# Kernel optimization log

Hardware: AMD Instinct MI355X
Metric: run time of the kernel (lower is better)

## Reference

```python
import jax, jax.numpy as jnp
import numpy as np

EPS_LN = 1e-5


def fwht(x):
    """Fast Walsh-Hadamard transform over the last axis (power-of-two length).
    Vectorized butterfly: log2(n) stages, each a reshape + add/sub."""
    orig_shape = x.shape
    n = orig_shape[-1]
    y = x.reshape(-1, n)
    h = 1
    while h < n:
        y = y.reshape(-1, n // (2 * h), 2, h)
        a = y[:, :, 0, :]
        b = y[:, :, 1, :]
        y = jnp.stack([a + b, a - b], axis=2).reshape(-1, n)
        h <<= 1
    return y.reshape(orig_shape)


def setup_inputs() -> dict:
    key = jax.random.key(0)
    kx, kw, kg = jax.random.split(key, 3)
    B, S, D_IN, D_OUT = 4, 4096, 2048, 2048
    x = jax.random.normal(kx, (B, S, D_IN), dtype=jnp.float32)
    # kaiming_uniform_(a=sqrt(5)) -> bound = 1/sqrt(in_features)
    bound = 1.0 / np.sqrt(D_IN)
    W = jax.random.uniform(kw, (D_OUT, D_IN), dtype=jnp.float32,
                           minval=-bound, maxval=bound)
    gamma = jnp.ones((D_IN,), dtype=jnp.float32)
    beta = jnp.zeros((D_IN,), dtype=jnp.float32)
    return {"x": x, "W": W, "gamma": gamma, "beta": beta}


def reference(x, W, gamma, beta):
    bits = 4
    max_val = (1 << (bits - 1)) - 1  # 7
    # LayerNorm over last dim
    mu = jnp.mean(x, axis=-1, keepdims=True)
    var = jnp.mean(jnp.square(x - mu), axis=-1, keepdims=True)
    x_ln = (x - mu) * jax.lax.rsqrt(var + EPS_LN) * gamma + beta
    # Activation fake-quant to `bits` bits (per-row absmax scale)
    x_scale = jnp.clip(jnp.max(jnp.abs(x_ln), axis=-1, keepdims=True), 1e-6, None)
    x_int = jnp.clip(jnp.round(x_ln * max_val / x_scale), -max_val, max_val)
    x_q = x_int * x_scale / max_val
    # Hadamard transform of quantized activations
    x_h = fwht(x_q)
    # Ternary weight quantization with global mean-abs scale
    w_scale = jnp.clip(jnp.mean(jnp.abs(W)), 1e-6, None)
    w_q = (jnp.where(W > 0.5 * w_scale, 1.0, 0.0)
           + jnp.where(W < -0.5 * w_scale, -1.0, 0.0)) * w_scale
    # Linear (no bias), then second Hadamard transform
    out = jnp.einsum('bsd,od->bso', x_h, w_q)
    return fwht(out)
```

## Files before the change

### kernel.cpp

```cpp
#include <hip/hip_runtime.h>

typedef unsigned short u16;
typedef __attribute__((ext_vector_type(8))) __bf16 bf16x8;
typedef __attribute__((ext_vector_type(4))) float floatx4;

#define DDIM 2048
#define MROWS 16384
#define BK 64

__device__ __forceinline__ u16 f2bf(float f) {
    unsigned int u = __builtin_bit_cast(unsigned int, f);
    u = (u + 0x7fffu + ((u >> 16) & 1u)) >> 16;
    return (u16)u;
}

__device__ __forceinline__ float wave_sum(float v) {
#pragma unroll
    for (int o = 32; o > 0; o >>= 1) v += __shfl_down(v, o, 64);
    return v;
}
__device__ __forceinline__ float wave_max(float v) {
#pragma unroll
    for (int o = 32; o > 0; o >>= 1) v = fmaxf(v, __shfl_down(v, o, 64));
    return v;
}

__global__ __launch_bounds__(256) void absmean_part(const float4* __restrict__ W4,
                                                    float* __restrict__ partial) {
    float s = 0.f;
    for (int i = blockIdx.x * 256 + threadIdx.x; i < (DDIM * DDIM / 4); i += 256 * 256) {
        float4 v = W4[i];
        s += fabsf(v.x) + fabsf(v.y) + fabsf(v.z) + fabsf(v.w);
    }
    s = wave_sum(s);
    __shared__ float red[4];
    if ((threadIdx.x & 63) == 0) red[threadIdx.x >> 6] = s;
    __syncthreads();
    if (threadIdx.x == 0) partial[blockIdx.x] = red[0] + red[1] + red[2] + red[3];
}

__global__ __launch_bounds__(256) void absmean_final(const float* __restrict__ partial,
                                                     float* __restrict__ scal) {
    float s = partial[threadIdx.x];
    s = wave_sum(s);
    __shared__ float red[4];
    if ((threadIdx.x & 63) == 0) red[threadIdx.x >> 6] = s;
    __syncthreads();
    if (threadIdx.x == 0) {
        float m = (red[0] + red[1] + red[2] + red[3]) * (1.0f / (float)(DDIM * DDIM));
        m = fmaxf(m, 1e-6f);
        scal[0] = m;
        scal[1] = 0.5f * m;
    }
}

template <bool QUANT>
__global__ __launch_bounds__(256) void transpose_k(const float* __restrict__ in,
                                                   float* __restrict__ out,
                                                   const float* __restrict__ scal) {
    __shared__ float tile[64][65];
    float wsc = 0.f, half_t = 0.f;
    if (QUANT) { wsc = scal[0]; half_t = scal[1]; }
    const int tx = threadIdx.x & 63;
    const int ty = threadIdx.x >> 6;
    const int r0 = blockIdx.y * 64;
    const int c0 = blockIdx.x * 64;
#pragma unroll
    for (int i = 0; i < 16; ++i) {
        int r = ty + i * 4;
        float w = in[(size_t)(r0 + r) * DDIM + c0 + tx];
        if (QUANT) w = (w > half_t ? wsc : 0.f) + (w < -half_t ? -wsc : 0.f);
        tile[r][tx] = w;
    }
    __syncthreads();
#pragma unroll
    for (int i = 0; i < 16; ++i) {
        int r = ty + i * 4;
        out[(size_t)(c0 + r) * DDIM + r0 + tx] = tile[tx][r];
    }
}

template <bool BF16OUT>
__global__ __launch_bounds__(256) void fwht_rows(const float* __restrict__ in,
                                                 void* __restrict__ out) {
    __shared__ float s0[DDIM];
    __shared__ float s1[DDIM];
    const int row = blockIdx.x;
    const int t = threadIdx.x;
    const int lane = t & 63;
    const float4* rp = (const float4*)(in + (size_t)row * DDIM);
    float4 a = rp[2 * t], b = rp[2 * t + 1];
    float v[8] = {a.x, a.y, a.z, a.w, b.x, b.y, b.z, b.w};

#pragma unroll
    for (int h = 1; h <= 4; h <<= 1)
#pragma unroll
        for (int j = 0; j < 8; ++j)
            if (!(j & h)) { float x = v[j], y = v[j | h]; v[j] = x + y; v[j | h] = x - y; }

#pragma unroll
    for (int m = 1; m <= 32; m <<= 1)
#pragma unroll
        for (int j = 0; j < 8; ++j) {
            float p = __shfl_xor(v[j], m, 64);
            v[j] = (lane & m) ? (p - v[j]) : (p + v[j]);
        }

    ((float4*)s0)[2 * t] = make_float4(v[0], v[1], v[2], v[3]);
    ((float4*)s0)[2 * t + 1] = make_float4(v[4], v[5], v[6], v[7]);
    __syncthreads();
    {
        int p1 = t ^ 64;
        float4 pa = ((const float4*)s0)[2 * p1], pb = ((const float4*)s0)[2 * p1 + 1];
        float pv[8] = {pa.x, pa.y, pa.z, pa.w, pb.x, pb.y, pb.z, pb.w};
#pragma unroll
        for (int j = 0; j < 8; ++j) v[j] = (t & 64) ? (pv[j] - v[j]) : (pv[j] + v[j]);
    }
    ((float4*)s1)[2 * t] = make_float4(v[0], v[1], v[2], v[3]);
    ((float4*)s1)[2 * t + 1] = make_float4(v[4], v[5], v[6], v[7]);
    __syncthreads();
    {
        int p2 = t ^ 128;
        float4 pa = ((const float4*)s1)[2 * p2], pb = ((const float4*)s1)[2 * p2 + 1];
        float pv[8] = {pa.x, pa.y, pa.z, pa.w, pb.x, pb.y, pb.z, pb.w};
#pragma unroll
        for (int j = 0; j < 8; ++j) v[j] = (t & 128) ? (pv[j] - v[j]) : (pv[j] + v[j]);
    }

    if (BF16OUT) {
        u16* op = (u16*)out + (size_t)row * DDIM;
        uint4 o;
        o.x = (unsigned)f2bf(v[0]) | ((unsigned)f2bf(v[1]) << 16);
        o.y = (unsigned)f2bf(v[2]) | ((unsigned)f2bf(v[3]) << 16);
        o.z = (unsigned)f2bf(v[4]) | ((unsigned)f2bf(v[5]) << 16);
        o.w = (unsigned)f2bf(v[6]) | ((unsigned)f2bf(v[7]) << 16);
        ((uint4*)op)[t] = o;
    } else {
        float* op = (float*)out + (size_t)row * DDIM;
        ((float4*)op)[2 * t] = make_float4(v[0], v[1], v[2], v[3]);
        ((float4*)op)[2 * t + 1] = make_float4(v[4], v[5], v[6], v[7]);
    }
}

__global__ __launch_bounds__(256) void ln_quant(const float* __restrict__ X,
                                                const float* __restrict__ G,
                                                const float* __restrict__ Bt,
                                                u16* __restrict__ XQ) {
    const int row = blockIdx.x;
    const int t = threadIdx.x;
    const float4* rp = (const float4*)(X + (size_t)row * DDIM);
    float4 v0 = rp[2 * t], v1 = rp[2 * t + 1];
    float v[8] = {v0.x, v0.y, v0.z, v0.w, v1.x, v1.y, v1.z, v1.w};

    __shared__ float redA[4], redB[4], redC[4];
    const int wv = t >> 6, ln = t & 63;

    float s = 0.f, s2 = 0.f;
#pragma unroll
    for (int j = 0; j < 8; ++j) { s += v[j]; s2 += v[j] * v[j]; }
#pragma unroll
    for (int o = 32; o > 0; o >>= 1) {
        s += __shfl_down(s, o, 64);
        s2 += __shfl_down(s2, o, 64);
    }
    if (ln == 0) { redA[wv] = s; redB[wv] = s2; }
    __syncthreads();
    const float mu = (redA[0] + redA[1] + redA[2] + redA[3]) * (1.f / (float)DDIM);
    const float ex2 = (redB[0] + redB[1] + redB[2] + redB[3]) * (1.f / (float)DDIM);
    const float var = ex2 - mu * mu;
    const float rstd = rsqrtf(var + 1e-5f);

    const float4* gp = (const float4*)G;
    const float4* bp = (const float4*)Bt;
    float4 g0 = gp[2 * t], g1 = gp[2 * t + 1];
    float4 b0 = bp[2 * t], b1 = bp[2 * t + 1];
    float gg[8] = {g0.x, g0.y, g0.z, g0.w, g1.x, g1.y, g1.z, g1.w};
    float bb[8] = {b0.x, b0.y, b0.z, b0.w, b1.x, b1.y, b1.z, b1.w};

    float y[8];
    float am = 0.f;
#pragma unroll
    for (int j = 0; j < 8; ++j) {
        y[j] = (v[j] - mu) * rstd * gg[j] + bb[j];
        am = fmaxf(am, fabsf(y[j]));
    }
    float w = wave_max(am);
    if (ln == 0) redC[wv] = w;
    __syncthreads();
    const float scale = fmaxf(fmaxf(fmaxf(redC[0], redC[1]), fmaxf(redC[2], redC[3])), 1e-6f);

    unsigned int q[4];
#pragma unroll
    for (int j = 0; j < 8; j += 2) {
        float qa = fminf(fmaxf(rintf(y[j] * 7.f / scale), -7.f), 7.f);
        float qb = fminf(fmaxf(rintf(y[j + 1] * 7.f / scale), -7.f), 7.f);
        q[j >> 1] = (unsigned)f2bf(qa * scale / 7.f) | ((unsigned)f2bf(qb * scale / 7.f) << 16);
    }
    uint4 o;
    o.x = q[0]; o.y = q[1]; o.z = q[2]; o.w = q[3];
    ((uint4*)(XQ + (size_t)row * DDIM))[t] = o;
}

__device__ __forceinline__ void gl_lds16(const u16* g, u16* l) {
    __builtin_amdgcn_global_load_lds((const __attribute__((address_space(1))) void*)g,
                                     (__attribute__((address_space(3))) void*)l,
                                     16, 0, 0);
}

__global__ __launch_bounds__(256) void gemm_bt(const u16* __restrict__ A,
                                               const u16* __restrict__ B,
                                               float* __restrict__ C) {
    __shared__ __align__(16) u16 As[128 * BK];
    __shared__ __align__(16) u16 Bs[128 * BK];
    const int bm = blockIdx.y, bn = blockIdx.x;
    const int t = threadIdx.x;
    const int wave = t >> 6, lane = t & 63;
    const int m_off = (wave >> 1) << 6;
    const int n_off = (wave & 1) << 6;
    const int lr = lane & 15, kq = lane >> 4;

    floatx4 acc[4][4];
#pragma unroll
    for (int i = 0; i < 4; ++i)
#pragma unroll
        for (int j = 0; j < 4; ++j) acc[i][j] = {0.f, 0.f, 0.f, 0.f};

    const int srow = t >> 3;
    const int sc = ((t & 7) ^ (srow & 7)) << 3;
    const u16* Ag = A + (size_t)(bm * 128 + srow) * DDIM + sc;
    const u16* Bg = B + (size_t)(bn * 128 + srow) * DDIM + sc;
    u16* Asl = As + t * 8;
    u16* Bsl = Bs + t * 8;

    for (int kt = 0; kt < DDIM / BK; ++kt) {
        const size_t ko = (size_t)kt * BK;
#pragma unroll
        for (int i = 0; i < 4; ++i) {
            gl_lds16(Ag + (size_t)(i * 32) * DDIM + ko, Asl + i * 2048);
            gl_lds16(Bg + (size_t)(i * 32) * DDIM + ko, Bsl + i * 2048);
        }
        __syncthreads();

#pragma unroll
        for (int s = 0; s < 2; ++s) {
            const int swz = ((kq + 4 * s) ^ (lr & 7)) << 3;
            bf16x8 af[4], bfr[4];
#pragma unroll
            for (int mi = 0; mi < 4; ++mi)
                af[mi] = *(const bf16x8*)(As + (m_off + mi * 16 + lr) * BK + swz);
#pragma unroll
            for (int ni = 0; ni < 4; ++ni)
                bfr[ni] = *(const bf16x8*)(Bs + (n_off + ni * 16 + lr) * BK + swz);
#pragma unroll
            for (int mi = 0; mi < 4; ++mi)
#pragma unroll
                for (int ni = 0; ni < 4; ++ni)
                    acc[mi][ni] = __builtin_amdgcn_mfma_f32_16x16x32_bf16(af[mi], bfr[ni],
                                                                          acc[mi][ni], 0, 0, 0);
        }
        __syncthreads();
    }

    const int mrow = kq * 4;
    float* Cb = C + (size_t)(bm * 128 + m_off) * DDIM + bn * 128 + n_off;
#pragma unroll
    for (int mi = 0; mi < 4; ++mi)
#pragma unroll
        for (int ni = 0; ni < 4; ++ni)
#pragma unroll
            for (int r = 0; r < 4; ++r)
                Cb[(size_t)(mi * 16 + mrow + r) * DDIM + ni * 16 + lr] = acc[mi][ni][r];
}

extern "C" void kernel_launch(void* const* d_in, const int* in_sizes, int n_in,
                              void* d_out, int out_size, void* d_ws, size_t ws_size,
                              hipStream_t stream) {
    const float* X  = (const float*)d_in[0];
    const float* W  = (const float*)d_in[1];
    const float* G  = (const float*)d_in[2];
    const float* Bt = (const float*)d_in[3];
    float* out = (float*)d_out;

    char* ws = (char*)d_ws;
    u16*   xq   = (u16*)ws;
    float* bufA = (float*)(ws + (size_t)67108864);
    float* bufB = (float*)(ws + (size_t)67108864 + 16777216);
    float* partial = bufB;
    float* scal    = bufB + 256;
    u16*   w3      = (u16*)bufB;

    absmean_part<<<256, 256, 0, stream>>>((const float4*)W, partial);
    absmean_final<<<1, 256, 0, stream>>>(partial, scal);
    transpose_k<true><<<dim3(32, 32), 256, 0, stream>>>(W, bufA, scal);
    fwht_rows<false><<<2048, 256, 0, stream>>>(bufA, (void*)bufB);
    transpose_k<false><<<dim3(32, 32), 256, 0, stream>>>(bufB, bufA, scal);
    fwht_rows<true><<<2048, 256, 0, stream>>>(bufA, (void*)w3);
    ln_quant<<<MROWS, 256, 0, stream>>>(X, G, Bt, xq);
    gemm_bt<<<dim3(DDIM / 128, MROWS / 128), 256, 0, stream>>>(xq, w3, out);
}
```

Before: 419.8 us.

## Swizzle GEMM block order, fuse absmean finalize, coalesce row loads and stores

Remaps GEMM block indices so that co-scheduled blocks share A and B tiles in cache. The single-block absmean_final kernel is folded into the quantizing transpose, which now reduces 1024 partial sums itself, and absmean_part is launched with more blocks. The fwht_rows and ln_quant kernels now read and write with a strided per-thread element layout (t and t+256) so accesses coalesce. This works because the FWHT is invariant to a consistent permutation of index bits. The cost is a redundant partial-sum reduction in every transpose block.

```diff
diff --git a/kernel.cpp b/kernel.cpp
--- a/kernel.cpp
+++ b/kernel.cpp
@@ -28,7 +28,7 @@
 __global__ __launch_bounds__(256) void absmean_part(const float4* __restrict__ W4,
                                                     float* __restrict__ partial) {
     float s = 0.f;
-    for (int i = blockIdx.x * 256 + threadIdx.x; i < (DDIM * DDIM / 4); i += 256 * 256) {
+    for (int i = blockIdx.x * 256 + threadIdx.x; i < (DDIM * DDIM / 4); i += 1024 * 256) {
         float4 v = W4[i];
         s += fabsf(v.x) + fabsf(v.y) + fabsf(v.z) + fabsf(v.w);
     }
@@ -39,30 +39,26 @@
     if (threadIdx.x == 0) partial[blockIdx.x] = red[0] + red[1] + red[2] + red[3];
 }
 
-__global__ __launch_bounds__(256) void absmean_final(const float* __restrict__ partial,
-                                                     float* __restrict__ scal) {
-    float s = partial[threadIdx.x];
-    s = wave_sum(s);
-    __shared__ float red[4];
-    if ((threadIdx.x & 63) == 0) red[threadIdx.x >> 6] = s;
-    __syncthreads();
-    if (threadIdx.x == 0) {
-        float m = (red[0] + red[1] + red[2] + red[3]) * (1.0f / (float)(DDIM * DDIM));
-        m = fmaxf(m, 1e-6f);
-        scal[0] = m;
-        scal[1] = 0.5f * m;
-    }
-}
-
 template <bool QUANT>
 __global__ __launch_bounds__(256) void transpose_k(const float* __restrict__ in,
                                                    float* __restrict__ out,
-                                                   const float* __restrict__ scal) {
+                                                   const float* __restrict__ partial) {
     __shared__ float tile[64][65];
+    const int t = threadIdx.x;
     float wsc = 0.f, half_t = 0.f;
-    if (QUANT) { wsc = scal[0]; half_t = scal[1]; }
-    const int tx = threadIdx.x & 63;
-    const int ty = threadIdx.x >> 6;
+    if (QUANT) {
+        __shared__ float wred[4];
+        float s = partial[t] + partial[t + 256] + partial[t + 512] + partial[t + 768];
+        s = wave_sum(s);
+        if ((t & 63) == 0) wred[t >> 6] = s;
+        __syncthreads();
+        float m = (wred[0] + wred[1] + wred[2] + wred[3]) * (1.0f / (float)(DDIM * DDIM));
+        wsc = fmaxf(m, 1e-6f);
+        half_t = 0.5f * wsc;
+        __syncthreads();
+    }
+    const int tx = t & 63;
+    const int ty = t >> 6;
     const int r0 = blockIdx.y * 64;
     const int c0 = blockIdx.x * 64;
 #pragma unroll
@@ -89,7 +85,7 @@
     const int t = threadIdx.x;
     const int lane = t & 63;
     const float4* rp = (const float4*)(in + (size_t)row * DDIM);
-    float4 a = rp[2 * t], b = rp[2 * t + 1];
+    float4 a = rp[t], b = rp[t + 256];
     float v[8] = {a.x, a.y, a.z, a.w, b.x, b.y, b.z, b.w};
 
 #pragma unroll
@@ -129,16 +125,17 @@
 
     if (BF16OUT) {
         u16* op = (u16*)out + (size_t)row * DDIM;
-        uint4 o;
-        o.x = (unsigned)f2bf(v[0]) | ((unsigned)f2bf(v[1]) << 16);
-        o.y = (unsigned)f2bf(v[2]) | ((unsigned)f2bf(v[3]) << 16);
-        o.z = (unsigned)f2bf(v[4]) | ((unsigned)f2bf(v[5]) << 16);
-        o.w = (unsigned)f2bf(v[6]) | ((unsigned)f2bf(v[7]) << 16);
-        ((uint4*)op)[t] = o;
+        uint2 o0, o1;
+        o0.x = (unsigned)f2bf(v[0]) | ((unsigned)f2bf(v[1]) << 16);
+        o0.y = (unsigned)f2bf(v[2]) | ((unsigned)f2bf(v[3]) << 16);
+        o1.x = (unsigned)f2bf(v[4]) | ((unsigned)f2bf(v[5]) << 16);
+        o1.y = (unsigned)f2bf(v[6]) | ((unsigned)f2bf(v[7]) << 16);
+        ((uint2*)op)[t] = o0;
+        ((uint2*)op)[t + 256] = o1;
     } else {
         float* op = (float*)out + (size_t)row * DDIM;
-        ((float4*)op)[2 * t] = make_float4(v[0], v[1], v[2], v[3]);
-        ((float4*)op)[2 * t + 1] = make_float4(v[4], v[5], v[6], v[7]);
+        ((float4*)op)[t] = make_float4(v[0], v[1], v[2], v[3]);
+        ((float4*)op)[t + 256] = make_float4(v[4], v[5], v[6], v[7]);
     }
 }
 
@@ -149,7 +146,7 @@
     const int row = blockIdx.x;
     const int t = threadIdx.x;
     const float4* rp = (const float4*)(X + (size_t)row * DDIM);
-    float4 v0 = rp[2 * t], v1 = rp[2 * t + 1];
+    float4 v0 = rp[t], v1 = rp[t + 256];
     float v[8] = {v0.x, v0.y, v0.z, v0.w, v1.x, v1.y, v1.z, v1.w};
 
     __shared__ float redA[4], redB[4], redC[4];
@@ -172,8 +169,8 @@
 
     const float4* gp = (const float4*)G;
     const float4* bp = (const float4*)Bt;
-    float4 g0 = gp[2 * t], g1 = gp[2 * t + 1];
-    float4 b0 = bp[2 * t], b1 = bp[2 * t + 1];
+    float4 g0 = gp[t], g1 = gp[t + 256];
+    float4 b0 = bp[t], b1 = bp[t + 256];
     float gg[8] = {g0.x, g0.y, g0.z, g0.w, g1.x, g1.y, g1.z, g1.w};
     float bb[8] = {b0.x, b0.y, b0.z, b0.w, b1.x, b1.y, b1.z, b1.w};
 
@@ -189,16 +186,19 @@
     __syncthreads();
     const float scale = fmaxf(fmaxf(fmaxf(redC[0], redC[1]), fmaxf(redC[2], redC[3])), 1e-6f);
 
+    const float r7 = 7.f / scale, s7 = scale / 7.f;
     unsigned int q[4];
 #pragma unroll
     for (int j = 0; j < 8; j += 2) {
-        float qa = fminf(fmaxf(rintf(y[j] * 7.f / scale), -7.f), 7.f);
-        float qb = fminf(fmaxf(rintf(y[j + 1] * 7.f / scale), -7.f), 7.f);
-        q[j >> 1] = (unsigned)f2bf(qa * scale / 7.f) | ((unsigned)f2bf(qb * scale / 7.f) << 16);
-    }
-    uint4 o;
-    o.x = q[0]; o.y = q[1]; o.z = q[2]; o.w = q[3];
-    ((uint4*)(XQ + (size_t)row * DDIM))[t] = o;
+        float qa = fminf(fmaxf(rintf(y[j] * r7), -7.f), 7.f);
+        float qb = fminf(fmaxf(rintf(y[j + 1] * r7), -7.f), 7.f);
+        q[j >> 1] = (unsigned)f2bf(qa * s7) | ((unsigned)f2bf(qb * s7) << 16);
+    }
+    uint2 o0, o1;
+    o0.x = q[0]; o0.y = q[1]; o1.x = q[2]; o1.y = q[3];
+    uint2* orow = (uint2*)(XQ + (size_t)row * DDIM);
+    orow[t] = o0;
+    orow[t + 256] = o1;
 }
 
 __device__ __forceinline__ void gl_lds16(const u16* g, u16* l) {
@@ -212,7 +212,9 @@
                                                float* __restrict__ C) {
     __shared__ __align__(16) u16 As[128 * BK];
     __shared__ __align__(16) u16 Bs[128 * BK];
-    const int bm = blockIdx.y, bn = blockIdx.x;
+    const int p = blockIdx.y * 16 + blockIdx.x;
+    const int bn = (p >> 3) & 15;
+    const int bm = (p & 7) * 16 + (p >> 7);
     const int t = threadIdx.x;
     const int wave = t >> 6, lane = t & 63;
     const int m_off = (wave >> 1) << 6;
@@ -286,15 +288,13 @@
     float* bufA = (float*)(ws + (size_t)67108864);
     float* bufB = (float*)(ws + (size_t)67108864 + 16777216);
     float* partial = bufB;
-    float* scal    = bufB + 256;
     u16*   w3      = (u16*)bufB;
 
-    absmean_part<<<256, 256, 0, stream>>>((const float4*)W, partial);
-    absmean_final<<<1, 256, 0, stream>>>(partial, scal);
-    transpose_k<true><<<dim3(32, 32), 256, 0, stream>>>(W, bufA, scal);
+    absmean_part<<<1024, 256, 0, stream>>>((const float4*)W, partial);
+    transpose_k<true><<<dim3(32, 32), 256, 0, stream>>>(W, bufA, partial);
     fwht_rows<false><<<2048, 256, 0, stream>>>(bufA, (void*)bufB);
-    transpose_k<false><<<dim3(32, 32), 256, 0, stream>>>(bufB, bufA, scal);
+    transpose_k<false><<<dim3(32, 32), 256, 0, stream>>>(bufB, bufA, nullptr);
     fwht_rows<true><<<2048, 256, 0, stream>>>(bufA, (void*)w3);
     ln_quant<<<MROWS, 256, 0, stream>>>(X, G, Bt, xq);
-    gemm_bt<<<dim3(DDIM / 128, MROWS / 128), 256, 0, stream>>>(xq, w3, out);
-}
+    gemm_bt<<<dim3(16, 128), 256, 0, stream>>>(xq, w3, out);
+}
```

After: 430.0 us. 2.4% more time.
